# Kernel tuning notes

Hardware: AMD Instinct MI355X
Metric: run time of the kernel (lower is better)

Reference implementation:

```python
import jax, jax.numpy as jnp
import numpy as np

EPS = 1e-05


def setup_inputs() -> dict:
    key = jax.random.key(0)
    x = jax.random.normal(key, (256, 256, 256), dtype=jnp.float32)
    return {"x": x}


def reference(x):
    # x: [B, N, N] dependency score logits
    B, N, _ = x.shape
    eye = jnp.eye(N, dtype=x.dtype)
    exp_x = jnp.exp(x)                                  # [B, N, N]
    diag_exp = jnp.exp(jnp.diagonal(x, axis1=-2, axis2=-1))  # [B, N] root scores

    # Build Laplacian: zero diagonal, negate off-diagonals, column sums on diag
    lap = (exp_x + EPS) * (1.0 - eye)                   # masked_fill diag with 0
    colsum = lap.sum(axis=-2)                           # torch sum(0) = column sums
    lap = -lap + colsum[:, None, :] * eye               # -lap + diag(colsum)
    # Replace row 0 with exp of the diagonal of input (root selection row)
    lap = lap.at[:, 0, :].set(diag_exp)

    inv = jnp.linalg.inv(lap)                           # batched inverse [B, N, N]
    d = jnp.diagonal(inv, axis1=-2, axis2=-1)           # [B, N]

    term1 = exp_x * d[:, None, :]                       # factor[i,j] = inv_diag[j]
    term2 = exp_x * jnp.swapaxes(inv, -1, -2)
    term1 = term1.at[:, :, 0].set(0.0)
    term2 = term2.at[:, 0, :].set(0.0)
    out = term1 - term2

    roots = diag_exp * inv[:, :, 0]                     # inv.T[0] == inv[:, 0]
    out = out + eye * roots[:, :, None]                 # add diag(roots)
    return out
```

## Files before the change

### kernel.cpp

```cpp
#include <hip/hip_runtime.h>
#include <math.h>

#define N 256
#define BS 32
#define NB_ 8
#define EPS 1e-5f

__global__ __launch_bounds__(1024) void mtt_fused(const float* __restrict__ x,
                                                  float* __restrict__ out) {
    constexpr int LDR = N + 8;
    __shared__ alignas(16) float  Rf[BS][LDR];
    __shared__ alignas(16) float  CfT[BS][LDR];
    __shared__ double Ps[BS][BS + 1];
    __shared__ double dsum[4][N];
    __shared__ float  sdiag_f[N];
    __shared__ float  sroot_f[N];
    __shared__ double spiv_s;
    __shared__ int    spidx_s;
    __shared__ int    indx[BS];

    const int tid = threadIdx.x;
    const int ty = tid >> 5, tx = tid & 31;
    const int R0  = ty << 3;
    const int c0a = tx << 2;
    const int c0b = 128 + (tx << 2);
    const int hibase = (ty >= 16) ? 4 : 0;
    const float* xb = x + (size_t)blockIdx.x * N * N;
    float* ob = out + (size_t)blockIdx.x * N * N;

    float m[8][8];

    double csacc = 0.0;
    const int tq = tid >> 8, jc = tid & 255;
    float exd[8];
    const bool needExd =
        (tx == 0) || (tx == ((2 * ty) & 31)) || (tx == ((2 * ty + 1) & 31));

#pragma unroll 1
    for (int s = 0; s < 8; ++s) {
        {
            const int cc0 = tx << 3;
            const float4 v0 = *(const float4*)&xb[(size_t)(32 * s + ty) * N + cc0];
            const float4 v1 = *(const float4*)&xb[(size_t)(32 * s + ty) * N + cc0 + 4];
            *(float4*)&Rf[ty][cc0]     = v0;
            *(float4*)&Rf[ty][cc0 + 4] = v1;
        }
        __syncthreads();
#pragma unroll
        for (int r = 0; r < 8; ++r) csacc += (double)expf(Rf[(tq << 3) + r][jc]);
        if ((tx >> 3) == s) {
            const int jb = (tx & 7) << 2;
#pragma unroll
            for (int cc = 0; cc < 4; ++cc)
#pragma unroll
                for (int r = 0; r < 8; ++r)
                    m[r][cc] = -(expf(Rf[jb + cc][R0 + r]) + EPS);
        }
        if (s >= 4 && (tx >> 3) == s - 4) {
            const int jb = (tx & 7) << 2;
#pragma unroll
            for (int cc = 0; cc < 4; ++cc)
#pragma unroll
                for (int r = 0; r < 8; ++r)
                    m[r][4 + cc] = -(expf(Rf[jb + cc][R0 + r]) + EPS);
        }
        if (needExd && (ty >> 2) == s) {
            const int base = R0 - (s << 5);
#pragma unroll
            for (int r = 0; r < 8; ++r) exd[r] = expf(Rf[base + r][R0 + r]);
        }
        __syncthreads();
    }
    dsum[tq][jc] = csacc;
    __syncthreads();
    if (tid < N)
        dsum[0][tid] = dsum[0][tid] + dsum[1][tid] + dsum[2][tid] + dsum[3][tid];
    __syncthreads();
#pragma unroll
    for (int r = 0; r < 8; ++r) {
        const int hb = r >> 2;
        if (tx == ((2 * ty + hb) & 31)) {
            const int i = R0 + r;
            if (i != 0)
                m[r][(r & 3) + hibase] =
                    (float)(dsum[0][i] - (double)exd[r] + 255.0 * (double)EPS);
        }
    }
    if (tx == 0) {
#pragma unroll
        for (int r = 0; r < 8; ++r) m[r][0] = exd[r];
    }

#pragma unroll 1
    for (int kb = 0; kb < NB_; ++kb) {
        const bool rowOwner = (ty >> 2) == kb;
        const bool h0piv = (kb < 4) && ((tx >> 3) == kb);
        const bool h1piv = (kb >= 4) && ((tx >> 3) == kb - 4);
        const int lr = (ty - (kb << 2)) << 3;
        const int lc = (tx & 7) << 2;

        if (rowOwner) {
#pragma unroll
            for (int r = 0; r < 8; ++r) {
                *(float4*)&Rf[lr + r][c0a] =
                    make_float4(m[r][0], m[r][1], m[r][2], m[r][3]);
                *(float4*)&Rf[lr + r][c0b] =
                    make_float4(m[r][4], m[r][5], m[r][6], m[r][7]);
            }
        }
        if (h0piv || h1piv) {
            const int cb = h0piv ? 0 : 4;
#pragma unroll
            for (int cc = 0; cc < 4; ++cc) {
                *(float4*)&CfT[lc + cc][R0] =
                    make_float4(m[0][cb + cc], m[1][cb + cc], m[2][cb + cc], m[3][cb + cc]);
                *(float4*)&CfT[lc + cc][R0 + 4] =
                    make_float4(m[4][cb + cc], m[5][cb + cc], m[6][cb + cc], m[7][cb + cc]);
            }
        }
        if (rowOwner && (h0piv || h1piv)) {
            const int cb = h0piv ? 0 : 4;
#pragma unroll
            for (int r = 0; r < 8; ++r)
#pragma unroll
                for (int cc = 0; cc < 4; ++cc)
                    Ps[lr + r][lc + cc] = (double)m[r][cb + cc];
        }
        __syncthreads();

        {
            const int r = ty, c = tx;
#pragma unroll 1
            for (int k2 = 0; k2 < BS; ++k2) {
                if (tid < 64) {
                    int rr = tid & 31;
                    double v  = Ps[rr][k2];
                    double av = (tid < 32 && rr >= k2) ? fabs(v) : -1.0;
                    int idx = rr;
                    for (int off = 16; off > 0; off >>= 1) {
                        double oav = __shfl_down(av, off);
                        double ov  = __shfl_down(v, off);
                        int    oi  = __shfl_down(idx, off);
                        if (oav > av) { av = oav; v = ov; idx = oi; }
                    }
                    if (tid == 0) { spidx_s = idx; spiv_s = 1.0 / v; indx[k2] = idx; }
                }
                __syncthreads();
                const int p = spidx_s;
                const double pivinv = spiv_s;
                const int sr = (r == k2) ? p : ((r == p) ? k2 : r);
                const double aval  = Ps[sr][c];
                const double prow  = Ps[p][c];
                const double scolr = Ps[sr][k2];
                __syncthreads();
                double nv;
                if (r == k2) {
                    nv = (c == k2) ? pivinv : prow * pivinv;
                } else {
                    const double srw  = (c == k2) ? pivinv : prow * pivinv;
                    const double base = (c == k2) ? 0.0 : aval;
                    nv = fma(-scolr, srw, base);
                }
                Ps[r][c] = nv;
                __syncthreads();
            }
            if (tid < 32) {
                for (int k2 = BS - 1; k2 >= 0; --k2) {
                    const int p = indx[k2];
                    if (p != k2) {
                        double t = Ps[tid][k2];
                        Ps[tid][k2] = Ps[tid][p];
                        Ps[tid][p]  = t;
                    }
                }
            }
            __syncthreads();
        }

        {
            double acc[8];
#pragma unroll
            for (int c = 0; c < 8; ++c) acc[c] = 0.0;
#pragma unroll 4
            for (int mm = 0; mm < BS; ++mm) {
                const double pv = Ps[ty][mm];
                const float4 r0 = *(const float4*)&Rf[mm][c0a];
                const float4 r1 = *(const float4*)&Rf[mm][c0b];
                acc[0] = fma(pv, (double)r0.x, acc[0]);
                acc[1] = fma(pv, (double)r0.y, acc[1]);
                acc[2] = fma(pv, (double)r0.z, acc[2]);
                acc[3] = fma(pv, (double)r0.w, acc[3]);
                acc[4] = fma(pv, (double)r1.x, acc[4]);
                acc[5] = fma(pv, (double)r1.y, acc[5]);
                acc[6] = fma(pv, (double)r1.z, acc[6]);
                acc[7] = fma(pv, (double)r1.w, acc[7]);
            }
            if (h0piv) {
#pragma unroll
                for (int cc = 0; cc < 4; ++cc) acc[cc] = Ps[ty][lc + cc];
            }
            if (h1piv) {
#pragma unroll
                for (int cc = 0; cc < 4; ++cc) acc[4 + cc] = Ps[ty][lc + cc];
            }
            __syncthreads();
            *(float4*)&Rf[ty][c0a] =
                make_float4((float)acc[0], (float)acc[1], (float)acc[2], (float)acc[3]);
            *(float4*)&Rf[ty][c0b] =
                make_float4((float)acc[4], (float)acc[5], (float)acc[6], (float)acc[7]);
        }
        __syncthreads();

        if (rowOwner) {
#pragma unroll
            for (int r = 0; r < 8; ++r) {
                const float4 a0 = *(const float4*)&Rf[lr + r][c0a];
                const float4 a1 = *(const float4*)&Rf[lr + r][c0b];
                m[r][0] = a0.x; m[r][1] = a0.y; m[r][2] = a0.z; m[r][3] = a0.w;
                m[r][4] = a1.x; m[r][5] = a1.y; m[r][6] = a1.z; m[r][7] = a1.w;
            }
        } else {
            if (h0piv) {
#pragma unroll
                for (int r = 0; r < 8; ++r) { m[r][0] = 0.f; m[r][1] = 0.f; m[r][2] = 0.f; m[r][3] = 0.f; }
            }
            if (h1piv) {
#pragma unroll
                for (int r = 0; r < 8; ++r) { m[r][4] = 0.f; m[r][5] = 0.f; m[r][6] = 0.f; m[r][7] = 0.f; }
            }
#pragma unroll 2
            for (int mm = 0; mm < BS; ++mm) {
                const float4 rv0 = *(const float4*)&Rf[mm][c0a];
                const float4 rv1 = *(const float4*)&Rf[mm][c0b];
                const float4 cv0 = *(const float4*)&CfT[mm][R0];
                const float4 cv1 = *(const float4*)&CfT[mm][R0 + 4];
                const float cr[8] = {-cv0.x, -cv0.y, -cv0.z, -cv0.w,
                                     -cv1.x, -cv1.y, -cv1.z, -cv1.w};
#pragma unroll
                for (int r = 0; r < 8; ++r) {
                    m[r][0] = fmaf(cr[r], rv0.x, m[r][0]);
                    m[r][1] = fmaf(cr[r], rv0.y, m[r][1]);
                    m[r][2] = fmaf(cr[r], rv0.z, m[r][2]);
                    m[r][3] = fmaf(cr[r], rv0.w, m[r][3]);
                    m[r][4] = fmaf(cr[r], rv1.x, m[r][4]);
                    m[r][5] = fmaf(cr[r], rv1.y, m[r][5]);
                    m[r][6] = fmaf(cr[r], rv1.z, m[r][6]);
                    m[r][7] = fmaf(cr[r], rv1.w, m[r][7]);
                }
            }
        }
        __syncthreads();
    }

#pragma unroll
    for (int r = 0; r < 8; ++r) {
        const int hb = r >> 2;
        if (tx == ((2 * ty + hb) & 31))
            sdiag_f[R0 + r] = m[r][(r & 3) + hibase];
    }
    if (ty == 0) {
        *(float4*)&sroot_f[c0a] = make_float4(m[0][0], m[0][1], m[0][2], m[0][3]);
        *(float4*)&sroot_f[c0b] = make_float4(m[0][4], m[0][5], m[0][6], m[0][7]);
    }
    __syncthreads();

    float sd[8];
    {
        const float4 s0 = *(const float4*)&sdiag_f[c0a];
        const float4 s1 = *(const float4*)&sdiag_f[c0b];
        sd[0] = s0.x; sd[1] = s0.y; sd[2] = s0.z; sd[3] = s0.w;
        sd[4] = s1.x; sd[5] = s1.y; sd[6] = s1.z; sd[7] = s1.w;
    }
#pragma unroll
    for (int r = 0; r < 8; ++r) {
        const int a = R0 + r;
        const float4 x0 = *(const float4*)&xb[(size_t)a * N + c0a];
        const float4 x1 = *(const float4*)&xb[(size_t)a * N + c0b];
        const float xv[8] = {x0.x, x0.y, x0.z, x0.w, x1.x, x1.y, x1.z, x1.w};
        const float rt = sroot_f[a];
        float ov[8];
#pragma unroll
        for (int c = 0; c < 8; ++c) {
            const int b_ = (c < 4) ? (c0a + c) : (c0b + (c - 4));
            const float e = expf(xv[c]);
            float o = (b_ == 0) ? 0.0f : e * sd[c];
            if (a != 0) o -= e * m[r][c];
            if (a == b_) o += e * rt;
            ov[c] = o;
        }
        *(float4*)&ob[(size_t)a * N + c0a] = make_float4(ov[0], ov[1], ov[2], ov[3]);
        *(float4*)&ob[(size_t)a * N + c0b] = make_float4(ov[4], ov[5], ov[6], ov[7]);
    }
}

extern "C" void kernel_launch(void* const* d_in, const int* in_sizes, int n_in,
                              void* d_out, int out_size, void* d_ws, size_t ws_size,
                              hipStream_t stream) {
    const float* x = (const float*)d_in[0];
    float* out = (float*)d_out;
    mtt_fused<<<256, 1024, 0, stream>>>(x, out);
}
```

Baseline: 508.6 us.

## Halve block size with 16 rows per thread and fp32 panel multiply

Shrinks the block from 1024 to 512 threads, so each thread now owns 16 rows of the 256x256 matrix in registers, and rescales every loop accordingly. Each wavefront now finds the pivot redundantly with xor shuffles, which removes one barrier and the shared broadcast per pivot step. The P·R panel multiply runs in fp32 instead of fp64, using a float copy of the inverted pivot block. The diagonal exponentials are gathered through a shared array. The aim is to cut barrier and fp64 costs, at the price of higher register pressure and lower accuracy in the panel multiply.

```diff
diff --git a/kernel.cpp b/kernel.cpp
--- a/kernel.cpp
+++ b/kernel.cpp
@@ -6,54 +6,52 @@
 #define NB_ 8
 #define EPS 1e-5f
 
-__global__ __launch_bounds__(1024) void mtt_fused(const float* __restrict__ x,
-                                                  float* __restrict__ out) {
+__global__ __launch_bounds__(512, 2) void mtt_fused(const float* __restrict__ x,
+                                                    float* __restrict__ out) {
     constexpr int LDR = N + 8;
     __shared__ alignas(16) float  Rf[BS][LDR];
     __shared__ alignas(16) float  CfT[BS][LDR];
     __shared__ double Ps[BS][BS + 1];
-    __shared__ double dsum[4][N];
+    __shared__ float  Pf[BS][BS + 1];
+    __shared__ double dsum[2][N];
+    __shared__ float  sdx[N];
     __shared__ float  sdiag_f[N];
     __shared__ float  sroot_f[N];
-    __shared__ double spiv_s;
-    __shared__ int    spidx_s;
     __shared__ int    indx[BS];
 
     const int tid = threadIdx.x;
     const int ty = tid >> 5, tx = tid & 31;
-    const int R0  = ty << 3;
+    const int R0  = ty << 4;
     const int c0a = tx << 2;
     const int c0b = 128 + (tx << 2);
-    const int hibase = (ty >= 16) ? 4 : 0;
     const float* xb = x + (size_t)blockIdx.x * N * N;
     float* ob = out + (size_t)blockIdx.x * N * N;
 
-    float m[8][8];
+    float m[16][8];
 
     double csacc = 0.0;
     const int tq = tid >> 8, jc = tid & 255;
-    float exd[8];
-    const bool needExd =
-        (tx == 0) || (tx == ((2 * ty) & 31)) || (tx == ((2 * ty + 1) & 31));
-
 #pragma unroll 1
     for (int s = 0; s < 8; ++s) {
         {
-            const int cc0 = tx << 3;
-            const float4 v0 = *(const float4*)&xb[(size_t)(32 * s + ty) * N + cc0];
-            const float4 v1 = *(const float4*)&xb[(size_t)(32 * s + ty) * N + cc0 + 4];
-            *(float4*)&Rf[ty][cc0]     = v0;
-            *(float4*)&Rf[ty][cc0 + 4] = v1;
-        }
-        __syncthreads();
-#pragma unroll
-        for (int r = 0; r < 8; ++r) csacc += (double)expf(Rf[(tq << 3) + r][jc]);
+            const int rl = tid >> 4, cl = (tid & 15) << 4;
+            const float* src = &xb[(size_t)(32 * s + rl) * N + cl];
+            *(float4*)&Rf[rl][cl]      = *(const float4*)&src[0];
+            *(float4*)&Rf[rl][cl + 4]  = *(const float4*)&src[4];
+            *(float4*)&Rf[rl][cl + 8]  = *(const float4*)&src[8];
+            *(float4*)&Rf[rl][cl + 12] = *(const float4*)&src[12];
+        }
+        __syncthreads();
+#pragma unroll
+        for (int r = 0; r < 16; ++r)
+            csacc += (double)expf(Rf[(tq << 4) + r][jc]);
+        if (tid < 32) sdx[32 * s + tid] = expf(Rf[tid][32 * s + tid]);
         if ((tx >> 3) == s) {
             const int jb = (tx & 7) << 2;
 #pragma unroll
             for (int cc = 0; cc < 4; ++cc)
 #pragma unroll
-                for (int r = 0; r < 8; ++r)
+                for (int r = 0; r < 16; ++r)
                     m[r][cc] = -(expf(Rf[jb + cc][R0 + r]) + EPS);
         }
         if (s >= 4 && (tx >> 3) == s - 4) {
@@ -61,107 +59,117 @@
 #pragma unroll
             for (int cc = 0; cc < 4; ++cc)
 #pragma unroll
-                for (int r = 0; r < 8; ++r)
+                for (int r = 0; r < 16; ++r)
                     m[r][4 + cc] = -(expf(Rf[jb + cc][R0 + r]) + EPS);
-        }
-        if (needExd && (ty >> 2) == s) {
-            const int base = R0 - (s << 5);
-#pragma unroll
-            for (int r = 0; r < 8; ++r) exd[r] = expf(Rf[base + r][R0 + r]);
         }
         __syncthreads();
     }
     dsum[tq][jc] = csacc;
     __syncthreads();
-    if (tid < N)
-        dsum[0][tid] = dsum[0][tid] + dsum[1][tid] + dsum[2][tid] + dsum[3][tid];
+    if (tid < N) dsum[0][tid] += dsum[1][tid];
     __syncthreads();
-#pragma unroll
-    for (int r = 0; r < 8; ++r) {
-        const int hb = r >> 2;
-        if (tx == ((2 * ty + hb) & 31)) {
+    if (ty < 8) {
+#pragma unroll
+        for (int r = 0; r < 16; ++r) {
             const int i = R0 + r;
-            if (i != 0)
-                m[r][(r & 3) + hibase] =
-                    (float)(dsum[0][i] - (double)exd[r] + 255.0 * (double)EPS);
+            if (tx == (i >> 2) && i != 0)
+                m[r][r & 3] =
+                    (float)(dsum[0][i] - (double)sdx[i] + 255.0 * (double)EPS);
+        }
+    } else {
+#pragma unroll
+        for (int r = 0; r < 16; ++r) {
+            const int i = R0 + r;
+            if (tx == ((i - 128) >> 2))
+                m[r][4 + (r & 3)] =
+                    (float)(dsum[0][i] - (double)sdx[i] + 255.0 * (double)EPS);
         }
     }
     if (tx == 0) {
 #pragma unroll
-        for (int r = 0; r < 8; ++r) m[r][0] = exd[r];
+        for (int r = 0; r < 16; ++r) m[r][0] = sdx[R0 + r];
     }
 
 #pragma unroll 1
     for (int kb = 0; kb < NB_; ++kb) {
-        const bool rowOwner = (ty >> 2) == kb;
+        const bool rowOwner = (ty >> 1) == kb;
         const bool h0piv = (kb < 4) && ((tx >> 3) == kb);
         const bool h1piv = (kb >= 4) && ((tx >> 3) == kb - 4);
-        const int lr = (ty - (kb << 2)) << 3;
+        const int lr = (ty - (kb << 1)) << 4;
         const int lc = (tx & 7) << 2;
 
         if (rowOwner) {
 #pragma unroll
-            for (int r = 0; r < 8; ++r) {
+            for (int r = 0; r < 16; ++r) {
                 *(float4*)&Rf[lr + r][c0a] =
                     make_float4(m[r][0], m[r][1], m[r][2], m[r][3]);
                 *(float4*)&Rf[lr + r][c0b] =
                     make_float4(m[r][4], m[r][5], m[r][6], m[r][7]);
             }
         }
-        if (h0piv || h1piv) {
-            const int cb = h0piv ? 0 : 4;
+        if (h0piv) {
 #pragma unroll
             for (int cc = 0; cc < 4; ++cc) {
-                *(float4*)&CfT[lc + cc][R0] =
-                    make_float4(m[0][cb + cc], m[1][cb + cc], m[2][cb + cc], m[3][cb + cc]);
-                *(float4*)&CfT[lc + cc][R0 + 4] =
-                    make_float4(m[4][cb + cc], m[5][cb + cc], m[6][cb + cc], m[7][cb + cc]);
-            }
-        }
-        if (rowOwner && (h0piv || h1piv)) {
-            const int cb = h0piv ? 0 : 4;
-#pragma unroll
-            for (int r = 0; r < 8; ++r)
-#pragma unroll
-                for (int cc = 0; cc < 4; ++cc)
-                    Ps[lr + r][lc + cc] = (double)m[r][cb + cc];
+                *(float4*)&CfT[lc + cc][R0]      = make_float4(m[0][cc],  m[1][cc],  m[2][cc],  m[3][cc]);
+                *(float4*)&CfT[lc + cc][R0 + 4]  = make_float4(m[4][cc],  m[5][cc],  m[6][cc],  m[7][cc]);
+                *(float4*)&CfT[lc + cc][R0 + 8]  = make_float4(m[8][cc],  m[9][cc],  m[10][cc], m[11][cc]);
+                *(float4*)&CfT[lc + cc][R0 + 12] = make_float4(m[12][cc], m[13][cc], m[14][cc], m[15][cc]);
+            }
+            if (rowOwner) {
+#pragma unroll
+                for (int r = 0; r < 16; ++r)
+#pragma unroll
+                    for (int cc = 0; cc < 4; ++cc)
+                        Ps[lr + r][lc + cc] = (double)m[r][cc];
+            }
+        }
+        if (h1piv) {
+#pragma unroll
+            for (int cc = 0; cc < 4; ++cc) {
+                *(float4*)&CfT[lc + cc][R0]      = make_float4(m[0][4+cc],  m[1][4+cc],  m[2][4+cc],  m[3][4+cc]);
+                *(float4*)&CfT[lc + cc][R0 + 4]  = make_float4(m[4][4+cc],  m[5][4+cc],  m[6][4+cc],  m[7][4+cc]);
+                *(float4*)&CfT[lc + cc][R0 + 8]  = make_float4(m[8][4+cc],  m[9][4+cc],  m[10][4+cc], m[11][4+cc]);
+                *(float4*)&CfT[lc + cc][R0 + 12] = make_float4(m[12][4+cc], m[13][4+cc], m[14][4+cc], m[15][4+cc]);
+            }
+            if (rowOwner) {
+#pragma unroll
+                for (int r = 0; r < 16; ++r)
+#pragma unroll
+                    for (int cc = 0; cc < 4; ++cc)
+                        Ps[lr + r][lc + cc] = (double)m[r][4 + cc];
+            }
         }
         __syncthreads();
 
         {
-            const int r = ty, c = tx;
+            const int rr = tid & 31;
+            const int r0 = ty, r1 = ty + 16, c = tx;
 #pragma unroll 1
             for (int k2 = 0; k2 < BS; ++k2) {
-                if (tid < 64) {
-                    int rr = tid & 31;
-                    double v  = Ps[rr][k2];
-                    double av = (tid < 32 && rr >= k2) ? fabs(v) : -1.0;
-                    int idx = rr;
-                    for (int off = 16; off > 0; off >>= 1) {
-                        double oav = __shfl_down(av, off);
-                        double ov  = __shfl_down(v, off);
-                        int    oi  = __shfl_down(idx, off);
-                        if (oav > av) { av = oav; v = ov; idx = oi; }
-                    }
-                    if (tid == 0) { spidx_s = idx; spiv_s = 1.0 / v; indx[k2] = idx; }
-                }
+                double v  = Ps[rr][k2];
+                double av = (rr >= k2) ? fabs(v) : -1.0;
+                int idx = rr;
+#pragma unroll
+                for (int off = 1; off < 64; off <<= 1) {
+                    const double oav = __shfl_xor(av, off);
+                    const double ov  = __shfl_xor(v, off);
+                    const int    oi  = __shfl_xor(idx, off);
+                    if (oav > av || (oav == av && oi < idx)) { av = oav; v = ov; idx = oi; }
+                }
+                const int p = idx;
+                const double pivinv = 1.0 / v;
+                if (tid == 0) indx[k2] = p;
+                const int sr0 = (r0 == k2) ? p : ((r0 == p) ? k2 : r0);
+                const int sr1 = (r1 == k2) ? p : ((r1 == p) ? k2 : r1);
+                const double prow  = Ps[p][c];
+                const double aval0 = Ps[sr0][c], scol0 = Ps[sr0][k2];
+                const double aval1 = Ps[sr1][c], scol1 = Ps[sr1][k2];
                 __syncthreads();
-                const int p = spidx_s;
-                const double pivinv = spiv_s;
-                const int sr = (r == k2) ? p : ((r == p) ? k2 : r);
-                const double aval  = Ps[sr][c];
-                const double prow  = Ps[p][c];
-                const double scolr = Ps[sr][k2];
-                __syncthreads();
-                double nv;
-                if (r == k2) {
-                    nv = (c == k2) ? pivinv : prow * pivinv;
-                } else {
-                    const double srw  = (c == k2) ? pivinv : prow * pivinv;
-                    const double base = (c == k2) ? 0.0 : aval;
-                    nv = fma(-scolr, srw, base);
-                }
-                Ps[r][c] = nv;
+                const double srw = (c == k2) ? pivinv : prow * pivinv;
+                const double b0  = (c == k2) ? 0.0 : aval0;
+                const double b1  = (c == k2) ? 0.0 : aval1;
+                Ps[r0][c] = (r0 == k2) ? srw : fma(-scol0, srw, b0);
+                Ps[r1][c] = (r1 == k2) ? srw : fma(-scol1, srw, b1);
                 __syncthreads();
             }
             if (tid < 32) {
@@ -175,58 +183,72 @@
                 }
             }
             __syncthreads();
+            Pf[ty][tx]      = (float)Ps[ty][tx];
+            Pf[ty + 16][tx] = (float)Ps[ty + 16][tx];
+            __syncthreads();
         }
 
         {
-            double acc[8];
-#pragma unroll
-            for (int c = 0; c < 8; ++c) acc[c] = 0.0;
-#pragma unroll 4
+            float a0[8], a1[8];
+#pragma unroll
+            for (int c = 0; c < 8; ++c) { a0[c] = 0.f; a1[c] = 0.f; }
+#pragma unroll 2
             for (int mm = 0; mm < BS; ++mm) {
-                const double pv = Ps[ty][mm];
+                const float p0 = Pf[ty][mm];
+                const float p1 = Pf[ty + 16][mm];
                 const float4 r0 = *(const float4*)&Rf[mm][c0a];
                 const float4 r1 = *(const float4*)&Rf[mm][c0b];
-                acc[0] = fma(pv, (double)r0.x, acc[0]);
-                acc[1] = fma(pv, (double)r0.y, acc[1]);
-                acc[2] = fma(pv, (double)r0.z, acc[2]);
-                acc[3] = fma(pv, (double)r0.w, acc[3]);
-                acc[4] = fma(pv, (double)r1.x, acc[4]);
-                acc[5] = fma(pv, (double)r1.y, acc[5]);
-                acc[6] = fma(pv, (double)r1.z, acc[6]);
-                acc[7] = fma(pv, (double)r1.w, acc[7]);
+                a0[0] = fmaf(p0, r0.x, a0[0]);  a1[0] = fmaf(p1, r0.x, a1[0]);
+                a0[1] = fmaf(p0, r0.y, a0[1]);  a1[1] = fmaf(p1, r0.y, a1[1]);
+                a0[2] = fmaf(p0, r0.z, a0[2]);  a1[2] = fmaf(p1, r0.z, a1[2]);
+                a0[3] = fmaf(p0, r0.w, a0[3]);  a1[3] = fmaf(p1, r0.w, a1[3]);
+                a0[4] = fmaf(p0, r1.x, a0[4]);  a1[4] = fmaf(p1, r1.x, a1[4]);
+                a0[5] = fmaf(p0, r1.y, a0[5]);  a1[5] = fmaf(p1, r1.y, a1[5]);
+                a0[6] = fmaf(p0, r1.z, a0[6]);  a1[6] = fmaf(p1, r1.z, a1[6]);
+                a0[7] = fmaf(p0, r1.w, a0[7]);  a1[7] = fmaf(p1, r1.w, a1[7]);
             }
             if (h0piv) {
 #pragma unroll
-                for (int cc = 0; cc < 4; ++cc) acc[cc] = Ps[ty][lc + cc];
+                for (int cc = 0; cc < 4; ++cc) {
+                    a0[cc] = Pf[ty][lc + cc];
+                    a1[cc] = Pf[ty + 16][lc + cc];
+                }
             }
             if (h1piv) {
 #pragma unroll
-                for (int cc = 0; cc < 4; ++cc) acc[4 + cc] = Ps[ty][lc + cc];
+                for (int cc = 0; cc < 4; ++cc) {
+                    a0[4 + cc] = Pf[ty][lc + cc];
+                    a1[4 + cc] = Pf[ty + 16][lc + cc];
+                }
             }
             __syncthreads();
-            *(float4*)&Rf[ty][c0a] =
-                make_float4((float)acc[0], (float)acc[1], (float)acc[2], (float)acc[3]);
-            *(float4*)&Rf[ty][c0b] =
-                make_float4((float)acc[4], (float)acc[5], (float)acc[6], (float)acc[7]);
+            *(float4*)&Rf[ty][c0a]      = make_float4(a0[0], a0[1], a0[2], a0[3]);
+            *(float4*)&Rf[ty][c0b]      = make_float4(a0[4], a0[5], a0[6], a0[7]);
+            *(float4*)&Rf[ty + 16][c0a] = make_float4(a1[0], a1[1], a1[2], a1[3]);
+            *(float4*)&Rf[ty + 16][c0b] = make_float4(a1[4], a1[5], a1[6], a1[7]);
         }
         __syncthreads();
 
         if (rowOwner) {
 #pragma unroll
-            for (int r = 0; r < 8; ++r) {
-                const float4 a0 = *(const float4*)&Rf[lr + r][c0a];
-                const float4 a1 = *(const float4*)&Rf[lr + r][c0b];
-                m[r][0] = a0.x; m[r][1] = a0.y; m[r][2] = a0.z; m[r][3] = a0.w;
-                m[r][4] = a1.x; m[r][5] = a1.y; m[r][6] = a1.z; m[r][7] = a1.w;
+            for (int r = 0; r < 16; ++r) {
+                const float4 b0 = *(const float4*)&Rf[lr + r][c0a];
+                const float4 b1 = *(const float4*)&Rf[lr + r][c0b];
+                m[r][0] = b0.x; m[r][1] = b0.y; m[r][2] = b0.z; m[r][3] = b0.w;
+                m[r][4] = b1.x; m[r][5] = b1.y; m[r][6] = b1.z; m[r][7] = b1.w;
             }
         } else {
             if (h0piv) {
 #pragma unroll
-                for (int r = 0; r < 8; ++r) { m[r][0] = 0.f; m[r][1] = 0.f; m[r][2] = 0.f; m[r][3] = 0.f; }
+                for (int r = 0; r < 16; ++r) {
+                    m[r][0] = 0.f; m[r][1] = 0.f; m[r][2] = 0.f; m[r][3] = 0.f;
+                }
             }
             if (h1piv) {
 #pragma unroll
-                for (int r = 0; r < 8; ++r) { m[r][4] = 0.f; m[r][5] = 0.f; m[r][6] = 0.f; m[r][7] = 0.f; }
+                for (int r = 0; r < 16; ++r) {
+                    m[r][4] = 0.f; m[r][5] = 0.f; m[r][6] = 0.f; m[r][7] = 0.f;
+                }
             }
 #pragma unroll 2
             for (int mm = 0; mm < BS; ++mm) {
@@ -234,29 +256,41 @@
                 const float4 rv1 = *(const float4*)&Rf[mm][c0b];
                 const float4 cv0 = *(const float4*)&CfT[mm][R0];
                 const float4 cv1 = *(const float4*)&CfT[mm][R0 + 4];
-                const float cr[8] = {-cv0.x, -cv0.y, -cv0.z, -cv0.w,
-                                     -cv1.x, -cv1.y, -cv1.z, -cv1.w};
-#pragma unroll
-                for (int r = 0; r < 8; ++r) {
-                    m[r][0] = fmaf(cr[r], rv0.x, m[r][0]);
-                    m[r][1] = fmaf(cr[r], rv0.y, m[r][1]);
-                    m[r][2] = fmaf(cr[r], rv0.z, m[r][2]);
-                    m[r][3] = fmaf(cr[r], rv0.w, m[r][3]);
-                    m[r][4] = fmaf(cr[r], rv1.x, m[r][4]);
-                    m[r][5] = fmaf(cr[r], rv1.y, m[r][5]);
-                    m[r][6] = fmaf(cr[r], rv1.z, m[r][6]);
-                    m[r][7] = fmaf(cr[r], rv1.w, m[r][7]);
-                }
-            }
-        }
-        __syncthreads();
-    }
-
-#pragma unroll
-    for (int r = 0; r < 8; ++r) {
-        const int hb = r >> 2;
-        if (tx == ((2 * ty + hb) & 31))
-            sdiag_f[R0 + r] = m[r][(r & 3) + hibase];
+                const float4 cv2 = *(const float4*)&CfT[mm][R0 + 8];
+                const float4 cv3 = *(const float4*)&CfT[mm][R0 + 12];
+                const float cc16[16] = {cv0.x, cv0.y, cv0.z, cv0.w,
+                                        cv1.x, cv1.y, cv1.z, cv1.w,
+                                        cv2.x, cv2.y, cv2.z, cv2.w,
+                                        cv3.x, cv3.y, cv3.z, cv3.w};
+#pragma unroll
+                for (int r = 0; r < 16; ++r) {
+                    const float cr = -cc16[r];
+                    m[r][0] = fmaf(cr, rv0.x, m[r][0]);
+                    m[r][1] = fmaf(cr, rv0.y, m[r][1]);
+                    m[r][2] = fmaf(cr, rv0.z, m[r][2]);
+                    m[r][3] = fmaf(cr, rv0.w, m[r][3]);
+                    m[r][4] = fmaf(cr, rv1.x, m[r][4]);
+                    m[r][5] = fmaf(cr, rv1.y, m[r][5]);
+                    m[r][6] = fmaf(cr, rv1.z, m[r][6]);
+                    m[r][7] = fmaf(cr, rv1.w, m[r][7]);
+                }
+            }
+        }
+        __syncthreads();
+    }
+
+    if (ty < 8) {
+#pragma unroll
+        for (int r = 0; r < 16; ++r) {
+            const int i = R0 + r;
+            if (tx == (i >> 2)) sdiag_f[i] = m[r][r & 3];
+        }
+    } else {
+#pragma unroll
+        for (int r = 0; r < 16; ++r) {
+            const int i = R0 + r;
+            if (tx == ((i - 128) >> 2)) sdiag_f[i] = m[r][4 + (r & 3)];
+        }
     }
     if (ty == 0) {
         *(float4*)&sroot_f[c0a] = make_float4(m[0][0], m[0][1], m[0][2], m[0][3]);
@@ -272,7 +306,7 @@
         sd[4] = s1.x; sd[5] = s1.y; sd[6] = s1.z; sd[7] = s1.w;
     }
 #pragma unroll
-    for (int r = 0; r < 8; ++r) {
+    for (int r = 0; r < 16; ++r) {
         const int a = R0 + r;
         const float4 x0 = *(const float4*)&xb[(size_t)a * N + c0a];
         const float4 x1 = *(const float4*)&xb[(size_t)a * N + c0b];
@@ -298,5 +332,5 @@
                               hipStream_t stream) {
     const float* x = (const float*)d_in[0];
     float* out = (float*)d_out;
-    mtt_fused<<<256, 1024, 0, stream>>>(x, out);
+    mtt_fused<<<256, 512, 0, stream>>>(x, out);
 }
```

After: 438.3 us. 13.8% less time.
